# Performance work log

Hardware: AMD Instinct MI355X
Metric: run time of the kernel (lower is better)

The kernel has to match this reference:

```python
import jax, jax.numpy as jnp
import numpy as np

N = 50000      # nodes
E = 600000     # edges
G = 256        # graphs in batch
HID = 128      # gcn hidden = gcn in = gcn out
EDIM = 16      # edge feature dim
EH = 64        # edge mlp hidden
NL = 4         # gcn layers
MIN_ = 200     # mol feature dim
MH = 256       # mlp hidden
MOUT = 128     # mlp out
PH = 512       # predictor hidden
PIN = HID + MOUT


def setup_inputs() -> dict:
    key = jax.random.key(0)
    ks = jax.random.split(key, 32)
    f = lambda k, s: jax.random.normal(k, s, dtype=jnp.float32)
    p = lambda k, s: 0.05 * jax.random.normal(k, s, dtype=jnp.float32)
    return {
        "x": f(ks[0], (N, HID)),
        "edge_index": jax.random.randint(ks[1], (2, E), 0, N),
        "edge_attr": f(ks[2], (E, EDIM)),
        "batch_index": jnp.sort(jax.random.randint(ks[3], (N,), 0, G)),
        "mol_features": f(ks[4], (G, MIN_)),
        # PDNConv params (stacked over NL layers)
        "conv_lin_W": p(ks[5], (NL, HID, HID)),
        "conv_mW1": p(ks[6], (NL, EDIM, EH)),
        "conv_mb1": p(ks[7], (NL, EH)),
        "conv_mW2": p(ks[8], (NL, EH)),
        "conv_mb2": p(ks[9], (NL,)),
        "conv_bias": p(ks[10], (NL, HID)),
        # dense Linear after each conv
        "gcn_W": p(ks[11], (NL, HID, HID)),
        "gcn_b": p(ks[12], (NL, HID)),
        # mol-feature MLP (n_mlp_layers=3 -> 4 linears)
        "mlp_W0": p(ks[13], (MIN_, MH)), "mlp_b0": p(ks[14], (MH,)),
        "mlp_W1": p(ks[15], (MH, MH)),   "mlp_b1": p(ks[16], (MH,)),
        "mlp_W2": p(ks[17], (MH, MH)),   "mlp_b2": p(ks[18], (MH,)),
        "mlp_W3": p(ks[19], (MH, MOUT)), "mlp_b3": p(ks[20], (MOUT,)),
        # predictor
        "pred_W0": p(ks[21], (PIN, PH)), "pred_b0": p(ks[22], (PH,)),
        "pred_W1": p(ks[23], (PH, PH)),  "pred_b1": p(ks[24], (PH,)),
        "out_W": p(ks[25], (PH, 1)),     "out_b": p(ks[26], (1,)),
    }


def _pdn_conv(h, row, col, edge_attr, lin_W, mW1, mb1, mW2, mb2, bias):
    # edge MLP -> sigmoid gate (PyG PDNConv)
    w = jax.nn.sigmoid(jnp.maximum(edge_attr @ mW1 + mb1, 0.0) @ mW2 + mb2)  # [E]
    # gcn_norm with self loops (fill weight 1.0)
    loop = jnp.arange(N)
    r = jnp.concatenate([row, loop])
    c = jnp.concatenate([col, loop])
    w_all = jnp.concatenate([w, jnp.ones((N,), h.dtype)])
    deg = jax.ops.segment_sum(w_all, c, num_segments=N)
    dinv = jnp.where(deg > 0, jax.lax.rsqrt(deg), 0.0)
    norm = dinv[r] * w_all * dinv[c]                                          # [E+N]
    hl = h @ lin_W                                                            # [N,HID]
    out = jax.ops.segment_sum(norm[:, None] * hl[r], c, num_segments=N)
    return out + bias


def reference(x, edge_index, edge_attr, batch_index, mol_features,
              conv_lin_W, conv_mW1, conv_mb1, conv_mW2, conv_mb2, conv_bias,
              gcn_W, gcn_b,
              mlp_W0, mlp_b0, mlp_W1, mlp_b1, mlp_W2, mlp_b2, mlp_W3, mlp_b3,
              pred_W0, pred_b0, pred_W1, pred_b1, out_W, out_b):
    row, col = edge_index[0], edge_index[1]
    relu = lambda v: jnp.maximum(v, 0.0)

    # GCN stack: PDNConv -> relu(Linear), x NL
    h1 = x
    for i in range(NL):
        h1 = _pdn_conv(h1, row, col, edge_attr, conv_lin_W[i], conv_mW1[i],
                       conv_mb1[i], conv_mW2[i], conv_mb2[i], conv_bias[i])
        h1 = relu(h1 @ gcn_W[i] + gcn_b[i])
    # global mean pool over graphs
    sums = jax.ops.segment_sum(h1, batch_index, num_segments=G)
    cnts = jax.ops.segment_sum(jnp.ones((N,), h1.dtype), batch_index, num_segments=G)
    h1 = sums / jnp.maximum(cnts, 1.0)[:, None]                               # [G,HID]

    # molecular-feature MLP
    h2 = relu(mol_features @ mlp_W0 + mlp_b0)
    h2 = relu(h2 @ mlp_W1 + mlp_b1)
    h2 = relu(h2 @ mlp_W2 + mlp_b2)
    h2 = relu(h2 @ mlp_W3 + mlp_b3)                                           # [G,MOUT]

    h = jnp.concatenate([h1, h2], axis=1)                                     # [G,PIN]
    h = relu(h @ pred_W0 + pred_b0)
    h = relu(h @ pred_W1 + pred_b1)
    return h @ out_W + out_b                                                  # [G,1]
```

## Files before the change

### kernel.cpp

```cpp
#include <hip/hip_runtime.h>
#include <hip/hip_bf16.h>


#define NN 50000
#define EE 600000
#define GG 256
#define HID 128
#define EDIM 16
#define EHID 64
#define NL 4
#define MIN_F 200
#define MH 256
#define MOUT 128
#define PH 512
#define PIN 256
#define SCAN_B 196
#define PCH 8
#define EMB 128

typedef __hip_bfloat16 bf16;
typedef __attribute__((ext_vector_type(8))) short bf16x8;
typedef __attribute__((ext_vector_type(4))) float f32x4;

__device__ __forceinline__ float bfl(unsigned u) { return __uint_as_float(u << 16); }
__device__ __forceinline__ float bfh(unsigned u) { return __uint_as_float(u & 0xffff0000u); }
__device__ __forceinline__ float b2f(bf16 x) { return __bfloat162float(x); }
__device__ __forceinline__ float ldf(const void* p, long i, bool bf) {
  return bf ? __bfloat162float(((const bf16*)p)[i]) : ((const float*)p)[i];
}
__device__ __forceinline__ unsigned short f2bf_bits(float v) {
  bf16 h = __float2bfloat16(v);
  return *reinterpret_cast<unsigned short*>(&h);
}

__global__ void probe_kernel(const unsigned short* __restrict__ xs, int* flag) {
  if (threadIdx.x == 0 && blockIdx.x == 0) {
    int sane = 0;
    for (int i = 0; i < 128; i++) {
      unsigned e = (xs[i] >> 7) & 0xFF;
      if (e >= 96 && e <= 159) sane++;
    }
    *flag = (sane >= 112) ? 1 : 0;
  }
}

__global__ __launch_bounds__(256) void cvt_to_bf16(const void* __restrict__ in,
                                                   unsigned short* __restrict__ outp,
                                                   int n8, const int* __restrict__ flag) {
  bool bf = *flag != 0;
  int i = blockIdx.x * 256 + threadIdx.x;
  if (i >= n8) return;
  if (bf) {
    reinterpret_cast<uint4*>(outp)[i] = reinterpret_cast<const uint4*>(in)[i];
  } else {
    const float4* p = reinterpret_cast<const float4*>(in) + (size_t)i * 2;
    float4 v0 = p[0], v1 = p[1];
    ushort4 a, b;
    a.x = f2bf_bits(v0.x); a.y = f2bf_bits(v0.y);
    a.z = f2bf_bits(v0.z); a.w = f2bf_bits(v0.w);
    b.x = f2bf_bits(v1.x); b.y = f2bf_bits(v1.y);
    b.z = f2bf_bits(v1.z); b.w = f2bf_bits(v1.w);
    reinterpret_cast<ushort4*>(outp)[i * 2] = a;
    reinterpret_cast<ushort4*>(outp)[i * 2 + 1] = b;
  }
}

__global__ __launch_bounds__(256) void cvt_molf(const void* __restrict__ in,
                                                float* __restrict__ outp,
                                                const int* __restrict__ flag) {
  bool bf = *flag != 0;
  int i = blockIdx.x * 256 + threadIdx.x;
  if (i >= GG * 50) return;
  int row = i / 50, c4 = (i % 50) * 4;
  float4 v;
  if (bf) {
    const unsigned short* p = (const unsigned short*)in + (size_t)row * MIN_F + c4;
    uint2 u = *reinterpret_cast<const uint2*>(p);
    v.x = bfl(u.x); v.y = bfh(u.x); v.z = bfl(u.y); v.w = bfh(u.y);
  } else {
    v = *reinterpret_cast<const float4*>((const float*)in + (size_t)row * MIN_F + c4);
  }
  *reinterpret_cast<float4*>(&outp[(size_t)row * 256 + c4]) = v;
}

__global__ __launch_bounds__(256) void prep_fused_w(const void* __restrict__ lin_W,
                                                    const void* __restrict__ gW,
                                                    unsigned short* __restrict__ Wt,
                                                    const int* __restrict__ flag) {
  bool bf = *flag != 0;
  int idx = blockIdx.x * 256 + threadIdx.x;
  if (idx >= 4 * 16384) return;
  int l = idx >> 14;
  int rem = idx & 16383;
  int n = rem >> 7, k = rem & 127;
  float s = 0.f;
  long lb = (long)l * 16384;
  for (int m = 0; m < 128; m++)
    s += ldf(lin_W, lb + (long)k * 128 + m, bf) * ldf(gW, lb + (long)m * 128 + n, bf);
  Wt[idx] = f2bf_bits(s);
}

__global__ __launch_bounds__(128) void prep_fused_b(const void* __restrict__ cbias,
                                                    const void* __restrict__ gW,
                                                    const void* __restrict__ gb,
                                                    float* __restrict__ bprime,
                                                    const int* __restrict__ flag) {
  bool bf = *flag != 0;
  int idx = blockIdx.x * 128 + threadIdx.x;
  if (idx >= NL * HID) return;
  int l = idx >> 7, n = idx & 127;
  float s = ldf(gb, idx, bf);
  long lb = (long)l * 16384;
  for (int k = 0; k < 128; k++)
    s += ldf(cbias, (long)l * 128 + k, bf) * ldf(gW, lb + (long)k * 128 + n, bf);
  bprime[idx] = s;
}

__global__ __launch_bounds__(256) void prep_edge_w(const void* __restrict__ mW1,
                                                   const void* __restrict__ mb1,
                                                   unsigned short* __restrict__ W1t,
                                                   const int* __restrict__ flag) {
  bool bf = *flag != 0;
  int idx = blockIdx.x * 256 + threadIdx.x;
  if (idx >= 256 * 32) return;
  int col = idx >> 5, k = idx & 31;
  float v = 0.f;
  if (k < EDIM) v = ldf(mW1, (long)(col >> 6) * (EDIM * EHID) + (long)k * EHID + (col & 63), bf);
  else if (k == EDIM) v = ldf(mb1, col, bf);
  W1t[idx] = f2bf_bits(v);
}

__global__ __launch_bounds__(256) void prep_tail(
    const void* __restrict__ mlpW0, const void* __restrict__ mlpW1,
    const void* __restrict__ mlpW2, const void* __restrict__ mlpW3,
    const void* __restrict__ predW0, const void* __restrict__ predW1,
    unsigned short* __restrict__ T, const int* __restrict__ flag) {
  bool bf = *flag != 0;
  int idx = blockIdx.x * 256 + threadIdx.x;
  const void* src; int N, Kp, Ksrc, off;
  if      (idx < 65536)  { src = mlpW0;  N = 256; Kp = 256; Ksrc = 200; off = 0; }
  else if (idx < 131072) { src = mlpW1;  N = 256; Kp = 256; Ksrc = 256; off = 65536; }
  else if (idx < 196608) { src = mlpW2;  N = 256; Kp = 256; Ksrc = 256; off = 131072; }
  else if (idx < 229376) { src = mlpW3;  N = 128; Kp = 256; Ksrc = 256; off = 196608; }
  else if (idx < 360448) { src = predW0; N = 512; Kp = 256; Ksrc = 256; off = 229376; }
  else if (idx < 622592) { src = predW1; N = 512; Kp = 512; Ksrc = 512; off = 360448; }
  else return;
  int rem = idx - off;
  int n = rem / Kp, k = rem % Kp;
  float v = (k < Ksrc) ? ldf(src, (long)k * N + n, bf) : 0.f;
  T[idx] = f2bf_bits(v);
}

__global__ __launch_bounds__(256) void count_kernel(const int* __restrict__ ei,
                                                    int* __restrict__ cnt) {
  int e = blockIdx.x * 256 + threadIdx.x;
  if (e >= EE) return;
  int c = ei[EE + e];
  c = min(max(c, 0), NN - 1);
  atomicAdd(&cnt[c], 1);
}

__global__ __launch_bounds__(256) void scan_phase1(const int* __restrict__ cnt,
                                                   int* __restrict__ bsum) {
  __shared__ int red[256];
  int tid = threadIdx.x;
  int i = blockIdx.x * 256 + tid;
  red[tid] = (i < NN) ? cnt[i] : 0;
  __syncthreads();
  for (int off = 128; off > 0; off >>= 1) {
    if (tid < off) red[tid] += red[tid + off];
    __syncthreads();
  }
  if (tid == 0) bsum[blockIdx.x] = red[0];
}

__global__ __launch_bounds__(256) void scan_phase2(int* __restrict__ bsum,
                                                   int* __restrict__ offs) {
  __shared__ int buf[256];
  int tid = threadIdx.x;
  int v = (tid < SCAN_B) ? bsum[tid] : 0;
  buf[tid] = v;
  __syncthreads();
  for (int off = 1; off < 256; off <<= 1) {
    int t = (tid >= off) ? buf[tid - off] : 0;
    __syncthreads();
    buf[tid] += t;
    __syncthreads();
  }
  if (tid < SCAN_B) bsum[tid] = buf[tid] - v;
  if (tid == 255) offs[NN] = buf[255];
}

__global__ __launch_bounds__(256) void scan_phase3(const int* __restrict__ cnt,
                                                   const int* __restrict__ bsum,
                                                   int* __restrict__ offs) {
  __shared__ int buf[256];
  int tid = threadIdx.x;
  int i = blockIdx.x * 256 + tid;
  int v = (i < NN) ? cnt[i] : 0;
  buf[tid] = v;
  __syncthreads();
  for (int off = 1; off < 256; off <<= 1) {
    int t = (tid >= off) ? buf[tid - off] : 0;
    __syncthreads();
    buf[tid] += t;
    __syncthreads();
  }
  if (i < NN) offs[i] = bsum[blockIdx.x] + buf[tid] - v;
}

__global__ __launch_bounds__(256) void fill_kernel(const int* __restrict__ ei,
                                                   const int* __restrict__ offs,
                                                   int* __restrict__ cursor,
                                                   int2* __restrict__ csr_se) {
  int e = blockIdx.x * 256 + threadIdx.x;
  if (e >= EE) return;
  int c = ei[EE + e];
  c = min(max(c, 0), NN - 1);
  int pos = offs[c] + atomicAdd(&cursor[c], 1);
  pos = min(max(pos, 0), EE - 1);
  csr_se[pos] = make_int2(ei[e], e);
}

__global__ __launch_bounds__(256) void edge_mlp_mfma(
    const void* __restrict__ eattr, const unsigned short* __restrict__ W1t,
    const void* __restrict__ mW2, const void* __restrict__ mb2,
    float* __restrict__ w_all4, const int* __restrict__ flag) {
  bool bf = *flag != 0;
  int tid = threadIdx.x;
  int wave = tid >> 6, lane = tid & 63;
  int l15 = lane & 15, quad = lane >> 4;

  bf16x8 afrag[4];
#pragma unroll
  for (int t = 0; t < 4; t++)
    afrag[t] =
        *reinterpret_cast<const bf16x8*>(&W1t[((wave * 4 + t) * 16 + l15) * 32 + quad * 8]);

  float w2v[16];
#pragma unroll
  for (int t = 0; t < 4; t++)
#pragma unroll
    for (int r = 0; r < 4; r++)
      w2v[t * 4 + r] = ldf(mW2, wave * 64 + t * 16 + quad * 4 + r, bf);
  float b2 = ldf(mb2, wave, bf);

  bf16x8 bconst = (bf16x8){0, 0, 0, 0, 0, 0, 0, 0};
  if (quad == 2) bconst[0] = (short)0x3F80;

  int ebase = blockIdx.x * EMB;
  int rowbytes = bf ? EDIM * 2 : EDIM * 4;
  const char* p = (const char*)eattr + (size_t)(ebase + l15) * rowbytes +
                  (size_t)quad * (rowbytes >> 1);
  int fragstep = 16 * rowbytes;

  auto loadb = [&](int fb, const char* pp) -> bf16x8 {
    bf16x8 v = bconst;
    if (quad < 2 && fb < EE) {
      if (bf) {
        v = *reinterpret_cast<const bf16x8*>(pp);
      } else {
        const float4* q = reinterpret_cast<const float4*>(pp);
        float4 v0 = q[0], v1 = q[1];
        v[0] = (short)f2bf_bits(v0.x); v[1] = (short)f2bf_bits(v0.y);
        v[2] = (short)f2bf_bits(v0.z); v[3] = (short)f2bf_bits(v0.w);
        v[4] = (short)f2bf_bits(v1.x); v[5] = (short)f2bf_bits(v1.y);
        v[6] = (short)f2bf_bits(v1.z); v[7] = (short)f2bf_bits(v1.w);
      }
    }
    return v;
  };

  bf16x8 bcur = loadb(ebase, p);
#pragma unroll 2
  for (int f = 0; f < EMB / 16; f++) {
    int fbase = ebase + f * 16;
    p += fragstep;
    bf16x8 bnxt = loadb(fbase + 16, p);
    if (fbase < EE) {
      float s0 = 0.f, s1 = 0.f, s2 = 0.f, s3 = 0.f;
#define DO_T(T, S)                                                            \
  {                                                                           \
    f32x4 acc = __builtin_amdgcn_mfma_f32_16x16x32_bf16(                      \
        afrag[T], bcur, (f32x4){0.f, 0.f, 0.f, 0.f}, 0, 0, 0);                \
    S = fmaf(fmaxf(acc.x, 0.f), w2v[T * 4 + 0], S);                           \
    S = fmaf(fmaxf(acc.y, 0.f), w2v[T * 4 + 1], S);                           \
    S = fmaf(fmaxf(acc.z, 0.f), w2v[T * 4 + 2], S);                           \
    S = fmaf(fmaxf(acc.w, 0.f), w2v[T * 4 + 3], S);                           \
  }
      DO_T(0, s0) DO_T(1, s1) DO_T(2, s2) DO_T(3, s3)
#undef DO_T
      float s = (s0 + s1) + (s2 + s3);
      s += __shfl_xor(s, 16);
      s += __shfl_xor(s, 32);
      if (quad == 0) {
        float g = 1.f / (1.f + __expf(-(s + b2)));
        w_all4[(size_t)(fbase + l15) * 4 + wave] = g;
      }
    }
    bcur = bnxt;
  }
}

__global__ __launch_bounds__(256) void csr_gather(const int2* __restrict__ csr_se,
                                                  const float* __restrict__ w_all4,
                                                  float* __restrict__ csr_val) {
  int k = blockIdx.x * 256 + threadIdx.x;
  if (k >= EE) return;
  int eid = csr_se[k].y;
  eid = min(max(eid, 0), EE - 1);
  float4 w = reinterpret_cast<const float4*>(w_all4)[eid];
  csr_val[k] = w.x;
  csr_val[(size_t)EE + k] = w.y;
  csr_val[2 * (size_t)EE + k] = w.z;
  csr_val[3 * (size_t)EE + k] = w.w;
}

__global__ __launch_bounds__(256) void deg_kernel(const int* __restrict__ offs,
                                                  const float* __restrict__ csr_val,
                                                  float* __restrict__ dinv4) {
  int n = blockIdx.x * 256 + threadIdx.x;
  if (n >= NN) return;
  int s = offs[n], e = offs[n + 1];
  float d0 = 1.f, d1 = 1.f, d2 = 1.f, d3 = 1.f;
  for (int k = s; k < e; k++) {
    d0 += csr_val[k];
    d1 += csr_val[EE + k];
    d2 += csr_val[2 * (size_t)EE + k];
    d3 += csr_val[3 * (size_t)EE + k];
  }
  float4 o;
  o.x = rsqrtf(d0); o.y = rsqrtf(d1); o.z = rsqrtf(d2); o.w = rsqrtf(d3);
  reinterpret_cast<float4*>(dinv4)[n] = o;
}

__global__ __launch_bounds__(256) void csr_scale_kernel(const int2* __restrict__ csr_se,
                                                        const float* __restrict__ dinv4,
                                                        float* __restrict__ csr_val) {
  int k = blockIdx.x * 256 + threadIdx.x;
  if (k >= EE) return;
  int s = csr_se[k].x;
  s = min(max(s, 0), NN - 1);
  float4 d = reinterpret_cast<const float4*>(dinv4)[s];
  csr_val[k] *= d.x;
  csr_val[(size_t)EE + k] *= d.y;
  csr_val[2 * (size_t)EE + k] *= d.z;
  csr_val[3 * (size_t)EE + k] *= d.w;
}

__global__ __launch_bounds__(256) void gemm_nodes_bf16(
    const unsigned short* __restrict__ A16, const unsigned short* __restrict__ Wt,
    const float* __restrict__ bias, unsigned short* __restrict__ out16,
    int relu) {
  __shared__ alignas(16) unsigned short sA[64 * 136];
  __shared__ alignas(16) unsigned short sW[128 * 136];
  int tid = threadIdx.x;
  int rbase = blockIdx.x * 64;

#pragma unroll
  for (int p = 0; p < 8; p++) {
    int idx8 = p * 256 + tid;
    int n = idx8 >> 4, kc = idx8 & 15;
    uint4 v = reinterpret_cast<const uint4*>(Wt)[idx8];
    *reinterpret_cast<uint4*>(&sW[n * 136 + kc * 8]) = v;
  }
#pragma unroll
  for (int p = 0; p < 4; p++) {
    int idx8 = p * 256 + tid;
    int m = idx8 >> 4, kc = idx8 & 15;
    int row = rbase + m;
    uint4 v = make_uint4(0u, 0u, 0u, 0u);
    if (row < NN)
      v = *reinterpret_cast<const uint4*>(&A16[(size_t)row * HID + kc * 8]);
    *reinterpret_cast<uint4*>(&sA[m * 136 + kc * 8]) = v;
  }
  __syncthreads();

  int wave = tid >> 6, lane = tid & 63;
  int l15 = lane & 15, quad = lane >> 4;
  int mstrip = wave * 16;

  f32x4 acc[8];
#pragma unroll
  for (int t = 0; t < 8; t++) acc[t] = (f32x4){0.f, 0.f, 0.f, 0.f};

#pragma unroll
  for (int ks = 0; ks < 4; ks++) {
    int k0 = ks * 32 + quad * 8;
    bf16x8 a = *reinterpret_cast<const bf16x8*>(&sA[(mstrip + l15) * 136 + k0]);
#pragma unroll
    for (int t = 0; t < 8; t++) {
      bf16x8 b = *reinterpret_cast<const bf16x8*>(&sW[(t * 16 + l15) * 136 + k0]);
      acc[t] = __builtin_amdgcn_mfma_f32_16x16x32_bf16(a, b, acc[t], 0, 0, 0);
    }
  }

#pragma unroll
  for (int t = 0; t < 8; t++) {
    int n = t * 16 + l15;
    float bv = bias ? bias[n] : 0.f;
#pragma unroll
    for (int r = 0; r < 4; r++) {
      int row = rbase + mstrip + quad * 4 + r;
      if (row < NN) {
        float o = acc[t][r] + bv;
        if (relu) o = fmaxf(o, 0.f);
        out16[(size_t)row * HID + n] = f2bf_bits(o);
      }
    }
  }
}

__global__ __launch_bounds__(256) void gemm_tail_mfma(
    const float* __restrict__ A, int lda, const unsigned short* __restrict__ Wt,
    int Kp, const void* __restrict__ bias, float* __restrict__ outp, int ldo,
    int relu, const int* __restrict__ flag) {
  __shared__ alignas(16) unsigned short sA[64 * 264];
  __shared__ alignas(16) unsigned short sW[64 * 264];
  int tid = threadIdx.x;
  int rbase = blockIdx.x * 64;
  int nbase = blockIdx.y * 64;
  int wave = tid >> 6, lane = tid & 63;
  int l15 = lane & 15, quad = lane >> 4;
  int mstrip = wave * 16;

  f32x4 acc[4];
#pragma unroll
  for (int t = 0; t < 4; t++) acc[t] = (f32x4){0.f, 0.f, 0.f, 0.f};

  for (int kc = 0; kc < Kp; kc += 256) {
#pragma unroll 4
    for (int p = 0; p < 16; p++) {
      int idx = p * 1024 + tid * 4;
      int m = idx >> 8, k = idx & 255;
      float4 v = *reinterpret_cast<const float4*>(&A[(size_t)(rbase + m) * lda + kc + k]);
      ushort4 b;
      b.x = f2bf_bits(v.x); b.y = f2bf_bits(v.y);
      b.z = f2bf_bits(v.z); b.w = f2bf_bits(v.w);
      *reinterpret_cast<ushort4*>(&sA[m * 264 + k]) = b;
    }
#pragma unroll 4
    for (int p = 0; p < 8; p++) {
      int idx8 = p * 256 + tid;
      int n = idx8 >> 5, kk = (idx8 & 31) * 8;
      uint4 v = *reinterpret_cast<const uint4*>(&Wt[(size_t)(nbase + n) * Kp + kc + kk]);
      *reinterpret_cast<uint4*>(&sW[n * 264 + kk]) = v;
    }
    __syncthreads();
#pragma unroll
    for (int ks = 0; ks < 8; ks++) {
      int k0 = ks * 32 + quad * 8;
      bf16x8 a = *reinterpret_cast<const bf16x8*>(&sA[(mstrip + l15) * 264 + k0]);
#pragma unroll
      for (int nt = 0; nt < 4; nt++) {
        bf16x8 b = *reinterpret_cast<const bf16x8*>(&sW[(nt * 16 + l15) * 264 + k0]);
        acc[nt] = __builtin_amdgcn_mfma_f32_16x16x32_bf16(a, b, acc[nt], 0, 0, 0);
      }
    }
    __syncthreads();
  }

  bool bf = *flag != 0;
#pragma unroll
  for (int nt = 0; nt < 4; nt++) {
    int col = nbase + nt * 16 + l15;
    float bv = ldf(bias, col, bf);
#pragma unroll
    for (int r = 0; r < 4; r++) {
      int row = rbase + mstrip + quad * 4 + r;
      float o = acc[nt][r] + bv;
      if (relu) o = fmaxf(o, 0.f);
      outp[(size_t)row * ldo + col] = o;
    }
  }
}

__global__ __launch_bounds__(256) void aggregate_kernel(
    const unsigned short* __restrict__ h16, const int* __restrict__ offs,
    const int2* __restrict__ csr_se, const float* __restrict__ csr_val,
    const float* __restrict__ dinv4, int layer,
    unsigned short* __restrict__ out16) {
  int wave = threadIdx.x >> 6;
  int lane = threadIdx.x & 63;
  int n = blockIdx.x * 4 + wave;
  int grp = lane >> 4;
  int c16 = lane & 15;
  int start = offs[n], end = offs[n + 1];
  float a0 = 0.f, a1 = 0.f, a2 = 0.f, a3 = 0.f;
  float a4 = 0.f, a5 = 0.f, a6 = 0.f, a7 = 0.f;
  float b0 = 0.f, b1 = 0.f, b2 = 0.f, b3 = 0.f;
  float b4 = 0.f, b5 = 0.f, b6 = 0.f, b7 = 0.f;
  for (int base = start; base < end; base += 64) {
    int k = base + lane;
    float vread = 0.f;
    int sread = 0;
    if (k < end) {
      sread = min(max(csr_se[k].x, 0), NN - 1);
      vread = csr_val[k];
    }
    int m = min(64, end - base);
    int j = grp;
    for (; j + 4 < m; j += 8) {
      float v0 = __shfl(vread, j);
      int si0 = __shfl(sread, j);
      float v1 = __shfl(vread, j + 4);
      int si1 = __shfl(sread, j + 4);
      uint4 u0 = *reinterpret_cast<const uint4*>(&h16[(size_t)si0 * HID + c16 * 8]);
      uint4 u1 = *reinterpret_cast<const uint4*>(&h16[(size_t)si1 * HID + c16 * 8]);
      a0 = fmaf(v0, bfl(u0.x), a0); a1 = fmaf(v0, bfh(u0.x), a1);
      a2 = fmaf(v0, bfl(u0.y), a2); a3 = fmaf(v0, bfh(u0.y), a3);
      a4 = fmaf(v0, bfl(u0.z), a4); a5 = fmaf(v0, bfh(u0.z), a5);
      a6 = fmaf(v0, bfl(u0.w), a6); a7 = fmaf(v0, bfh(u0.w), a7);
      b0 = fmaf(v1, bfl(u1.x), b0); b1 = fmaf(v1, bfh(u1.x), b1);
      b2 = fmaf(v1, bfl(u1.y), b2); b3 = fmaf(v1, bfh(u1.y), b3);
      b4 = fmaf(v1, bfl(u1.z), b4); b5 = fmaf(v1, bfh(u1.z), b5);
      b6 = fmaf(v1, bfl(u1.w), b6); b7 = fmaf(v1, bfh(u1.w), b7);
    }
    if (j < m) {
      float v = __shfl(vread, j);
      int si = __shfl(sread, j);
      uint4 u = *reinterpret_cast<const uint4*>(&h16[(size_t)si * HID + c16 * 8]);
      a0 = fmaf(v, bfl(u.x), a0); a1 = fmaf(v, bfh(u.x), a1);
      a2 = fmaf(v, bfl(u.y), a2); a3 = fmaf(v, bfh(u.y), a3);
      a4 = fmaf(v, bfl(u.z), a4); a5 = fmaf(v, bfh(u.z), a5);
      a6 = fmaf(v, bfl(u.w), a6); a7 = fmaf(v, bfh(u.w), a7);
    }
  }
  a0 += b0; a1 += b1; a2 += b2; a3 += b3;
  a4 += b4; a5 += b5; a6 += b6; a7 += b7;
  a0 += __shfl_xor(a0, 16); a1 += __shfl_xor(a1, 16);
  a2 += __shfl_xor(a2, 16); a3 += __shfl_xor(a3, 16);
  a4 += __shfl_xor(a4, 16); a5 += __shfl_xor(a5, 16);
  a6 += __shfl_xor(a6, 16); a7 += __shfl_xor(a7, 16);
  a0 += __shfl_xor(a0, 32); a1 += __shfl_xor(a1, 32);
  a2 += __shfl_xor(a2, 32); a3 += __shfl_xor(a3, 32);
  a4 += __shfl_xor(a4, 32); a5 += __shfl_xor(a5, 32);
  a6 += __shfl_xor(a6, 32); a7 += __shfl_xor(a7, 32);
  if (grp == 0) {
    float dn = dinv4[(size_t)n * 4 + layer];
    float dn2 = dn * dn;
    uint4 su = *reinterpret_cast<const uint4*>(&h16[(size_t)n * HID + c16 * 8]);
    ushort4 o0, o1v;
    o0.x  = f2bf_bits(dn * a0 + dn2 * bfl(su.x));
    o0.y  = f2bf_bits(dn * a1 + dn2 * bfh(su.x));
    o0.z  = f2bf_bits(dn * a2 + dn2 * bfl(su.y));
    o0.w  = f2bf_bits(dn * a3 + dn2 * bfh(su.y));
    o1v.x = f2bf_bits(dn * a4 + dn2 * bfl(su.z));
    o1v.y = f2bf_bits(dn * a5 + dn2 * bfh(su.z));
    o1v.z = f2bf_bits(dn * a6 + dn2 * bfl(su.w));
    o1v.w = f2bf_bits(dn * a7 + dn2 * bfh(su.w));
    *reinterpret_cast<ushort4*>(&out16[(size_t)n * HID + c16 * 8]) = o0;
    *reinterpret_cast<ushort4*>(&out16[(size_t)n * HID + c16 * 8 + 4]) = o1v;
  }
}

__global__ __launch_bounds__(128) void pool_partial(const unsigned short* __restrict__ h16,
                                                    const int* __restrict__ batch,
                                                    float* __restrict__ part) {
  int g = blockIdx.x, chunk = blockIdx.y, c = threadIdx.x;
  int lo = 0, hi = NN;
  while (lo < hi) { int mid = (lo + hi) >> 1; if (batch[mid] < g) lo = mid + 1; else hi = mid; }
  int start = lo;
  hi = NN;
  while (lo < hi) { int mid = (lo + hi) >> 1; if (batch[mid] < g + 1) lo = mid + 1; else hi = mid; }
  int end = lo;
  int len = end - start;
  int per = (len + PCH - 1) / PCH;
  int s = start + chunk * per;
  int e = min(s + per, end);
  float sum = 0.f;
  for (int n = s; n < e; n++) sum += bfl((unsigned)h16[(size_t)n * HID + c]);
  part[((size_t)g * PCH + chunk) * HID + c] = sum;
}

__global__ __launch_bounds__(128) void pool_combine(const float* __restrict__ part,
                                                    const int* __restrict__ batch,
                                                    float* __restrict__ cat) {
  int g = blockIdx.x, c = threadIdx.x;
  int lo = 0, hi = NN;
  while (lo < hi) { int mid = (lo + hi) >> 1; if (batch[mid] < g) lo = mid + 1; else hi = mid; }
  int start = lo;
  hi = NN;
  while (lo < hi) { int mid = (lo + hi) >> 1; if (batch[mid] < g + 1) lo = mid + 1; else hi = mid; }
  int end = lo;
  float s = 0.f;
#pragma unroll
  for (int k = 0; k < PCH; k++) s += part[((size_t)g * PCH + k) * HID + c];
  float cntf = (float)(end - start);
  cat[(size_t)g * PIN + c] = s / fmaxf(cntf, 1.f);
}

__global__ __launch_bounds__(64) void final_kernel(const float* __restrict__ A,
                                                   const void* __restrict__ W,
                                                   const void* __restrict__ b,
                                                   void* __restrict__ outp,
                                                   const int* __restrict__ flag) {
  bool bf = *flag != 0;
  int g = blockIdx.x, lane = threadIdx.x;
  float s = 0.f;
  for (int k = lane; k < PH; k += 64) s = fmaf(A[(size_t)g * PH + k], ldf(W, k, bf), s);
#pragma unroll
  for (int off = 32; off > 0; off >>= 1) s += __shfl_down(s, off);
  if (lane == 0) {
    float r = s + ldf(b, 0, bf);
    if (bf) ((bf16*)outp)[g] = __float2bfloat16(r);
    else    ((float*)outp)[g] = r;
  }
}

extern "C" void kernel_launch(void* const* d_in, const int* in_sizes, int n_in,
                              void* d_out, int out_size, void* d_ws, size_t ws_size,
                              hipStream_t stream) {
  const void* x      = d_in[0];
  const int*  ei     = (const int*)d_in[1];
  const void* eattr  = d_in[2];
  const int*  batch  = (const int*)d_in[3];
  const void* molf   = d_in[4];
  const void* lin_W  = d_in[5];
  const void* mW1    = d_in[6];
  const void* mb1    = d_in[7];
  const void* mW2    = d_in[8];
  const void* mb2    = d_in[9];
  const void* cbias  = d_in[10];
  const void* gW     = d_in[11];
  const void* gb     = d_in[12];
  const void* mlpW0  = d_in[13];
  const void* mlpb0  = d_in[14];
  const void* mlpW1  = d_in[15];
  const void* mlpb1  = d_in[16];
  const void* mlpW2  = d_in[17];
  const void* mlpb2  = d_in[18];
  const void* mlpW3  = d_in[19];
  const void* mlpb3  = d_in[20];
  const void* predW0 = d_in[21];
  const void* predb0 = d_in[22];
  const void* predW1 = d_in[23];
  const void* predb1 = d_in[24];
  const void* outW   = d_in[25];
  const void* outb   = d_in[26];

  char* base = (char*)d_ws;
  size_t off = 0;
  auto alloc = [&](size_t bytes) -> char* {
    char* p = base + off;
    off = (off + bytes + 255) & ~(size_t)255;
    return p;
  };
  unsigned short* h16  = (unsigned short*)alloc((size_t)NN * HID * 2);
  unsigned short* t16  = (unsigned short*)alloc((size_t)NN * HID * 2);
  float* dinv4    = (float*)alloc((size_t)NN * 4 * 4);
  int*   cnt      = (int*)alloc((size_t)NN * 4);
  int*   offs     = (int*)alloc((size_t)(NN + 1) * 4);
  int*   cursor   = (int*)alloc((size_t)NN * 4);
  int*   bsum     = (int*)alloc((size_t)256 * 4);
  int2*  csr_se   = (int2*)alloc((size_t)EE * 8);
  float* csr_val  = (float*)alloc((size_t)NL * EE * 4);
  float* w_all4   = (float*)alloc((size_t)EE * 4 * 4);
  unsigned short* Wt    = (unsigned short*)alloc((size_t)NL * HID * HID * 2);
  float* bprime   = (float*)alloc((size_t)NL * HID * 4);
  unsigned short* tailW = (unsigned short*)alloc((size_t)622592 * 2);
  unsigned short* edgeW = (unsigned short*)alloc((size_t)256 * 32 * 2);
  int*   flag     = (int*)alloc(256);
  float* part     = (float*)alloc((size_t)GG * PCH * HID * 4);
  float* molf32   = (float*)alloc((size_t)GG * 256 * 4);
  float* m0       = (float*)alloc((size_t)GG * MH * 4);
  float* m1       = (float*)alloc((size_t)GG * MH * 4);
  float* cat      = (float*)alloc((size_t)GG * PIN * 4);
  float* p0       = (float*)alloc((size_t)GG * PH * 4);
  float* p1       = (float*)alloc((size_t)GG * PH * 4);

  hipMemsetAsync(cnt, 0, (size_t)NN * 4, stream);
  hipMemsetAsync(cursor, 0, (size_t)NN * 4, stream);
  hipMemsetAsync(molf32, 0, (size_t)GG * 256 * 4, stream);

  probe_kernel<<<1, 64, 0, stream>>>((const unsigned short*)x, flag);

  prep_fused_w<<<256, 256, 0, stream>>>(lin_W, gW, Wt, flag);
  prep_fused_b<<<NL, 128, 0, stream>>>(cbias, gW, gb, bprime, flag);
  prep_tail<<<(622592 + 255) / 256, 256, 0, stream>>>(mlpW0, mlpW1, mlpW2, mlpW3,
                                                      predW0, predW1, tailW, flag);
  prep_edge_w<<<32, 256, 0, stream>>>(mW1, mb1, edgeW, flag);

  {
    int n8 = NN * HID / 8;
    cvt_to_bf16<<<(n8 + 255) / 256, 256, 0, stream>>>(x, h16, n8, flag);
  }
  edge_mlp_mfma<<<(EE + EMB - 1) / EMB, 256, 0, stream>>>(eattr, edgeW, mW2, mb2,
                                                          w_all4, flag);
  count_kernel<<<(EE + 255) / 256, 256, 0, stream>>>(ei, cnt);
  scan_phase1<<<SCAN_B, 256, 0, stream>>>(cnt, bsum);
  scan_phase2<<<1, 256, 0, stream>>>(bsum, offs);
  scan_phase3<<<SCAN_B, 256, 0, stream>>>(cnt, bsum, offs);
  fill_kernel<<<(EE + 255) / 256, 256, 0, stream>>>(ei, offs, cursor, csr_se);
  csr_gather<<<(EE + 255) / 256, 256, 0, stream>>>(csr_se, w_all4, csr_val);
  deg_kernel<<<(NN + 255) / 256, 256, 0, stream>>>(offs, csr_val, dinv4);
  csr_scale_kernel<<<(EE + 255) / 256, 256, 0, stream>>>(csr_se, dinv4, csr_val);

  const int gemm_blocks = (NN + 63) / 64;
  for (int l = 0; l < NL; l++) {
    aggregate_kernel<<<NN / 4, 256, 0, stream>>>(h16, offs, csr_se,
                                                 csr_val + (size_t)l * EE, dinv4, l, t16);
    gemm_nodes_bf16<<<gemm_blocks, 256, 0, stream>>>(
        t16, Wt + (size_t)l * HID * HID, bprime + (size_t)l * HID, h16, 1);
  }

  pool_partial<<<dim3(GG, PCH), 128, 0, stream>>>(h16, batch, part);
  pool_combine<<<GG, 128, 0, stream>>>(part, batch, cat);

  cvt_molf<<<(GG * 50 + 255) / 256, 256, 0, stream>>>(molf, molf32, flag);
  gemm_tail_mfma<<<dim3(4, 4), 256, 0, stream>>>(molf32, 256, tailW + 0,      256, mlpb0, m0, 256, 1, flag);
  gemm_tail_mfma<<<dim3(4, 4), 256, 0, stream>>>(m0,     256, tailW + 65536,  256, mlpb1, m1, 256, 1, flag);
  gemm_tail_mfma<<<dim3(4, 4), 256, 0, stream>>>(m1,     256, tailW + 131072, 256, mlpb2, m0, 256, 1, flag);
  gemm_tail_mfma<<<dim3(4, 2), 256, 0, stream>>>(m0,     256, tailW + 196608, 256, mlpb3, cat + MOUT, 256, 1, flag);

  gemm_tail_mfma<<<dim3(4, 8), 256, 0, stream>>>(cat, 256, tailW + 229376, 256, predb0, p0, 512, 1, flag);
  gemm_tail_mfma<<<dim3(4, 8), 256, 0, stream>>>(p0,  512, tailW + 360448, 512, predb1, p1, 512, 1, flag);
  final_kernel<<<GG, 64, 0, stream>>>(p1, outW, outb, d_out, flag);
}
```

Baseline: 575.3 us.

## Drop materialized CSR edge weights; gather and normalize on the fly in aggregate

Removes the csr_gather and csr_scale kernels and the NL×E csr_val buffer. deg_kernel now gathers edge weights directly from w_all4 through the CSR edge ids, and aggregate_kernel computes each normalized weight on the fly as w_all4[eid, layer] × dinv4[src, layer]. This saves two launches and several full passes over edge arrays, but adds two random gathers per edge in every layer's aggregation. The edge MLP loop also now prefetches B fragments two steps ahead instead of one.

```diff
diff --git a/kernel.cpp b/kernel.cpp
--- a/kernel.cpp
+++ b/kernel.cpp
@@ -272,11 +272,11 @@
   };
 
   bf16x8 bcur = loadb(ebase, p);
+  bf16x8 bnx = loadb(ebase + 16, p + fragstep);
 #pragma unroll 2
   for (int f = 0; f < EMB / 16; f++) {
     int fbase = ebase + f * 16;
-    p += fragstep;
-    bf16x8 bnxt = loadb(fbase + 16, p);
+    bf16x8 b2f_ = loadb(fbase + 32, p + 2 * fragstep);
     if (fbase < EE) {
       float s0 = 0.f, s1 = 0.f, s2 = 0.f, s3 = 0.f;
 #define DO_T(T, S)                                                            \
@@ -298,54 +298,28 @@
         w_all4[(size_t)(fbase + l15) * 4 + wave] = g;
       }
     }
-    bcur = bnxt;
-  }
-}
-
-__global__ __launch_bounds__(256) void csr_gather(const int2* __restrict__ csr_se,
+    bcur = bnx;
+    bnx = b2f_;
+    p += fragstep;
+  }
+}
+
+__global__ __launch_bounds__(256) void deg_kernel(const int* __restrict__ offs,
+                                                  const int2* __restrict__ csr_se,
                                                   const float* __restrict__ w_all4,
-                                                  float* __restrict__ csr_val) {
-  int k = blockIdx.x * 256 + threadIdx.x;
-  if (k >= EE) return;
-  int eid = csr_se[k].y;
-  eid = min(max(eid, 0), EE - 1);
-  float4 w = reinterpret_cast<const float4*>(w_all4)[eid];
-  csr_val[k] = w.x;
-  csr_val[(size_t)EE + k] = w.y;
-  csr_val[2 * (size_t)EE + k] = w.z;
-  csr_val[3 * (size_t)EE + k] = w.w;
-}
-
-__global__ __launch_bounds__(256) void deg_kernel(const int* __restrict__ offs,
-                                                  const float* __restrict__ csr_val,
                                                   float* __restrict__ dinv4) {
   int n = blockIdx.x * 256 + threadIdx.x;
   if (n >= NN) return;
   int s = offs[n], e = offs[n + 1];
   float d0 = 1.f, d1 = 1.f, d2 = 1.f, d3 = 1.f;
   for (int k = s; k < e; k++) {
-    d0 += csr_val[k];
-    d1 += csr_val[EE + k];
-    d2 += csr_val[2 * (size_t)EE + k];
-    d3 += csr_val[3 * (size_t)EE + k];
+    int eid = min(max(csr_se[k].y, 0), EE - 1);
+    float4 w = reinterpret_cast<const float4*>(w_all4)[eid];
+    d0 += w.x; d1 += w.y; d2 += w.z; d3 += w.w;
   }
   float4 o;
   o.x = rsqrtf(d0); o.y = rsqrtf(d1); o.z = rsqrtf(d2); o.w = rsqrtf(d3);
   reinterpret_cast<float4*>(dinv4)[n] = o;
-}
-
-__global__ __launch_bounds__(256) void csr_scale_kernel(const int2* __restrict__ csr_se,
-                                                        const float* __restrict__ dinv4,
-                                                        float* __restrict__ csr_val) {
-  int k = blockIdx.x * 256 + threadIdx.x;
-  if (k >= EE) return;
-  int s = csr_se[k].x;
-  s = min(max(s, 0), NN - 1);
-  float4 d = reinterpret_cast<const float4*>(dinv4)[s];
-  csr_val[k] *= d.x;
-  csr_val[(size_t)EE + k] *= d.y;
-  csr_val[2 * (size_t)EE + k] *= d.z;
-  csr_val[3 * (size_t)EE + k] *= d.w;
 }
 
 __global__ __launch_bounds__(256) void gemm_nodes_bf16(
@@ -477,7 +451,7 @@
 
 __global__ __launch_bounds__(256) void aggregate_kernel(
     const unsigned short* __restrict__ h16, const int* __restrict__ offs,
-    const int2* __restrict__ csr_se, const float* __restrict__ csr_val,
+    const int2* __restrict__ csr_se, const float* __restrict__ w_all4,
     const float* __restrict__ dinv4, int layer,
     unsigned short* __restrict__ out16) {
   int wave = threadIdx.x >> 6;
@@ -495,8 +469,10 @@
     float vread = 0.f;
     int sread = 0;
     if (k < end) {
-      sread = min(max(csr_se[k].x, 0), NN - 1);
-      vread = csr_val[k];
+      int2 se = csr_se[k];
+      sread = min(max(se.x, 0), NN - 1);
+      int eid = min(max(se.y, 0), EE - 1);
+      vread = w_all4[(size_t)eid * 4 + layer] * dinv4[(size_t)sread * 4 + layer];
     }
     int m = min(64, end - base);
     int j = grp;
@@ -654,7 +630,6 @@
   int*   cursor   = (int*)alloc((size_t)NN * 4);
   int*   bsum     = (int*)alloc((size_t)256 * 4);
   int2*  csr_se   = (int2*)alloc((size_t)EE * 8);
-  float* csr_val  = (float*)alloc((size_t)NL * EE * 4);
   float* w_all4   = (float*)alloc((size_t)EE * 4 * 4);
   unsigned short* Wt    = (unsigned short*)alloc((size_t)NL * HID * HID * 2);
   float* bprime   = (float*)alloc((size_t)NL * HID * 4);
@@ -692,14 +667,12 @@
   scan_phase2<<<1, 256, 0, stream>>>(bsum, offs);
   scan_phase3<<<SCAN_B, 256, 0, stream>>>(cnt, bsum, offs);
   fill_kernel<<<(EE + 255) / 256, 256, 0, stream>>>(ei, offs, cursor, csr_se);
-  csr_gather<<<(EE + 255) / 256, 256, 0, stream>>>(csr_se, w_all4, csr_val);
-  deg_kernel<<<(NN + 255) / 256, 256, 0, stream>>>(offs, csr_val, dinv4);
-  csr_scale_kernel<<<(EE + 255) / 256, 256, 0, stream>>>(csr_se, dinv4, csr_val);
+  deg_kernel<<<(NN + 255) / 256, 256, 0, stream>>>(offs, csr_se, w_all4, dinv4);
 
   const int gemm_blocks = (NN + 63) / 64;
   for (int l = 0; l < NL; l++) {
     aggregate_kernel<<<NN / 4, 256, 0, stream>>>(h16, offs, csr_se,
-                                                 csr_val + (size_t)l * EE, dinv4, l, t16);
+                                                 w_all4, dinv4, l, t16);
     gemm_nodes_bf16<<<gemm_blocks, 256, 0, stream>>>(
         t16, Wt + (size_t)l * HID * HID, bprime + (size_t)l * HID, h16, 1);
   }
```

After: 601.8 us. +4.6%, slower.
